# Kernel tuning notes

Measured on AMD Instinct MI355X. Metric: run time of the kernel, lower is better.

## Reference

```python
import jax, jax.numpy as jnp
import numpy as np

USER_NUM = 100000
ITEM_NUM = 100000
N_NODES = USER_NUM + ITEM_NUM
EMB = 64
N_EDGES = 6400000
N_LAYERS = 3
LAYER_CL = 1
EPS = 0.1


def setup_inputs() -> dict:
    key = jax.random.key(0)
    k1, k2, k3, k4, k5, k6 = jax.random.split(key, 6)
    # Xavier-uniform-like scale for embeddings
    scale = float(np.sqrt(6.0 / (USER_NUM + EMB)))
    user_emb = jax.random.normal(k1, (USER_NUM, EMB), dtype=jnp.float32) * scale
    item_emb = jax.random.normal(k2, (ITEM_NUM, EMB), dtype=jnp.float32) * scale
    adj_rows = jax.random.randint(k3, (N_EDGES,), 0, N_NODES, dtype=jnp.int64)
    adj_cols = jax.random.randint(k4, (N_EDGES,), 0, N_NODES, dtype=jnp.int64)
    # normalized adjacency values ~ 1/degree
    adj_vals = jax.random.uniform(k5, (N_EDGES,), dtype=jnp.float32) * (1.0 / 32.0)
    # precomputed uniform noise replacing torch.rand_like per layer
    noise = jax.random.uniform(k6, (N_LAYERS, N_NODES, EMB), dtype=jnp.float32)
    return {"user_emb": user_emb, "item_emb": item_emb, "adj_rows": adj_rows,
            "adj_cols": adj_cols, "adj_vals": adj_vals, "noise": noise}


def _spmm(rows, cols, vals, x):
    # sparse [N,N] @ dense [N,D] via gather + segment_sum
    return jax.ops.segment_sum(vals[:, None] * x[cols], rows, num_segments=N_NODES)


def reference(user_emb, item_emb, adj_rows, adj_cols, adj_vals, noise):
    ego = jnp.concatenate([user_emb, item_emb], axis=0)  # [N, D]
    cl = ego
    acc = jnp.zeros_like(ego)
    for k in range(N_LAYERS):
        ego = _spmm(adj_rows, adj_cols, adj_vals, ego)
        # perturbed branch: ego += sign(ego) * F.normalize(noise_k, dim=-1) * eps
        nk = noise[k]
        nrm = jnp.maximum(jnp.linalg.norm(nk, axis=-1, keepdims=True), 1e-12)
        ego = ego + jnp.sign(ego) * (nk / nrm) * EPS
        acc = acc + ego
        if k == LAYER_CL - 1:
            cl = ego
    final = acc / N_LAYERS  # mean over stacked layer outputs
    return (final[:USER_NUM], final[USER_NUM:], cl[:USER_NUM], cl[USER_NUM:])
```

## Files before the change

### kernel.cpp

```cpp
#include <hip/hip_runtime.h>


#define USER_NUM 100000
#define N_NODES  200000
#define EMB      64
#define N_EDGES  6400000
#define NBUCK    782
#define CAP      9216
#define EPB      16384
#define TB_A     1024
#define NBLK     391

static constexpr size_t BUFA_OFF  = 0;
static constexpr size_t BUFB_OFF  = 51200000;
static constexpr size_t CV_OFF    = 102400000;
static constexpr size_t RS_OFF    = 153600000;
static constexpr size_t SMALL_OFF = 154400016;
static constexpr size_t WS_NEED   = 156000016;

typedef float f4v __attribute__((ext_vector_type(4)));

__device__ __forceinline__ float4 ntload4(const float* p) {
    f4v v = __builtin_nontemporal_load((const f4v*)p);
    return make_float4(v.x, v.y, v.z, v.w);
}
__device__ __forceinline__ void ntstore4(float* p, float4 v) {
    f4v t = {v.x, v.y, v.z, v.w};
    __builtin_nontemporal_store(t, (f4v*)p);
}

__global__ __launch_bounds__(TB_A) void k_prep(const int* __restrict__ rows,
                                               const int* __restrict__ cols,
                                               const float* __restrict__ vals,
                                               int* __restrict__ bcnt_part,
                                               int2* __restrict__ zip) {
    __shared__ int h[NBUCK];
    for (int i = threadIdx.x; i < NBUCK; i += TB_A) h[i] = 0;
    __syncthreads();
    int base = blockIdx.x * EPB;
    int end  = min(base + EPB, N_EDGES);
    for (int e = base + threadIdx.x; e < end; e += TB_A) {
        atomicAdd(&h[rows[e] >> 8], 1);
        zip[e] = make_int2(cols[e], __float_as_int(vals[e]));
    }
    __syncthreads();
    for (int i = threadIdx.x; i < NBUCK; i += TB_A)
        bcnt_part[blockIdx.x * NBUCK + i] = h[i];
}

__global__ void k_scan782(const int* __restrict__ bcnt_part,
                          int* __restrict__ bcnt, int* __restrict__ bbase,
                          int* __restrict__ gcur, int* __restrict__ rs) {
    __shared__ int s[1024];
    int i = threadIdx.x;
    int v = 0;
    if (i < NBUCK) {
        for (int b = 0; b < NBLK; ++b) v += bcnt_part[b * NBUCK + i];
        bcnt[i] = v;
    }
    s[i] = v;
    __syncthreads();
    for (int off = 1; off < 1024; off <<= 1) {
        int t = 0;
        if (i >= off) t = s[i - off];
        __syncthreads();
        s[i] += t;
        __syncthreads();
    }
    if (i < NBUCK) {
        int ex = s[i] - v;
        bbase[i] = ex;
        gcur[i] = ex;
    }
    if (i == 0) rs[N_NODES] = N_EDGES;
}

__global__ __launch_bounds__(TB_A) void k_bin(const int* __restrict__ rows,
                                              int* __restrict__ gcur,
                                              int* __restrict__ keys) {
    __shared__ int h[NBUCK];
    __shared__ int gb[NBUCK];
    for (int i = threadIdx.x; i < NBUCK; i += TB_A) h[i] = 0;
    __syncthreads();
    int base = blockIdx.x * EPB;
    int end  = min(base + EPB, N_EDGES);
    for (int e = base + threadIdx.x; e < end; e += TB_A)
        atomicAdd(&h[rows[e] >> 8], 1);
    __syncthreads();
    for (int i = threadIdx.x; i < NBUCK; i += TB_A) {
        int c = h[i];
        gb[i] = c ? atomicAdd(&gcur[i], c) : 0;
        h[i] = 0;
    }
    __syncthreads();
    for (int e = base + threadIdx.x; e < end; e += TB_A) {
        int r = rows[e];
        int b = r >> 8;
        int pos = gb[b] + atomicAdd(&h[b], 1);
        keys[pos] = ((r & 255) << 24) | e;
    }
}

__global__ __launch_bounds__(256) void k_build(const int* __restrict__ keys,
                                               const int2* __restrict__ zip,
                                               const int* __restrict__ bcnt,
                                               const int* __restrict__ bbase,
                                               int2* __restrict__ cv,
                                               int* __restrict__ rs) {
    __shared__ int cnt[256];
    __shared__ int start[256];
    __shared__ int cur[256];
    __shared__ int scanbuf[256];
    __shared__ int eKey[CAP];
    int tid = threadIdx.x;
    int b = blockIdx.x;
    int n = bcnt[b];
    int base = bbase[b];
    int rowbase = b << 8;
    cnt[tid] = 0;
    __syncthreads();
    for (int i = tid; i < n; i += 256) {
        unsigned key = (unsigned)keys[base + i];
        atomicAdd(&cnt[key >> 24], 1);
    }
    __syncthreads();
    int v = cnt[tid];
    scanbuf[tid] = v;
    __syncthreads();
    for (int off = 1; off < 256; off <<= 1) {
        int t = 0;
        if (tid >= off) t = scanbuf[tid - off];
        __syncthreads();
        scanbuf[tid] += t;
        __syncthreads();
    }
    start[tid] = scanbuf[tid] - v;
    {
        int row = rowbase + tid;
        if (row < N_NODES) rs[row] = base + start[tid];
    }
    cur[tid] = 0;
    __syncthreads();
    if (n <= CAP) {
        for (int i = tid; i < n; i += 256) {
            int key = keys[base + i];
            int rl = (int)((unsigned)key >> 24);
            int p = start[rl] + atomicAdd(&cur[rl], 1);
            eKey[p] = key;
        }
        __syncthreads();
        for (int p = tid; p < n; p += 256) {
            int k = eKey[p];
            int rl = (int)((unsigned)k >> 24);
            int s0 = start[rl];
            int s1 = s0 + cnt[rl];
            int rank = 0;
            int q = s0;
            for (; q + 4 <= s1; q += 4) {
                rank += (eKey[q]     < k);
                rank += (eKey[q + 1] < k);
                rank += (eKey[q + 2] < k);
                rank += (eKey[q + 3] < k);
            }
            for (; q < s1; ++q) rank += (eKey[q] < k);
            int e = k & 0x00FFFFFF;
            cv[base + s0 + rank] = zip[e];
        }
    } else {
        for (int i = tid; i < n; i += 256) {
            int key = keys[base + i];
            int rl = (int)((unsigned)key >> 24);
            int p = start[rl] + atomicAdd(&cur[rl], 1);
            cv[base + p] = make_int2(key, 0);
        }
        __syncthreads();
        int c = cnt[tid];
        if (c > 1) {
            int s0 = start[tid];
            int s1 = s0 + c;
            for (int i = s0 + 1; i < s1; ++i) {
                int2 kv = cv[base + i];
                int j = i - 1;
                while (j >= s0 && cv[base + j].x > kv.x) {
                    cv[base + j + 1] = cv[base + j];
                    --j;
                }
                cv[base + j + 1] = kv;
            }
        }
        __syncthreads();
        for (int i = tid; i < n; i += 256) {
            int e = cv[base + i].x & 0x00FFFFFF;
            cv[base + i] = zip[e];
        }
    }
}

__global__ __launch_bounds__(256) void k_fused(const int* __restrict__ rs,
                                               const int2* __restrict__ cv,
                                               const float* __restrict__ xlo,
                                               const float* __restrict__ xhi,
                                               int split,
                                               const float* __restrict__ nk,
                                               float* __restrict__ ego,
                                               float* __restrict__ accF,
                                               float* __restrict__ clF,
                                               int mode) {
    int t = blockIdx.x * blockDim.x + threadIdx.x;
    int r = t >> 4;
    int u = t & 15;
    int c = u << 2;
    int idx = t << 2;
    float4 n4 = ntload4(nk + idx);
    float q0 = __fmul_rn(n4.x, n4.x);
    float q1 = __fmul_rn(n4.y, n4.y);
    float q2 = __fmul_rn(n4.z, n4.z);
    float q3 = __fmul_rn(n4.w, n4.w);
    float f0 = q0, f1 = q1, f2 = q2, f3 = q3;
    #pragma unroll
    for (int s = 0; s < 7; ++s) {
        float g0 = __shfl_up(f0, 2, 16);
        float g1 = __shfl_up(f1, 2, 16);
        float g2 = __shfl_up(f2, 2, 16);
        float g3 = __shfl_up(f3, 2, 16);
        if (u >= 2) {
            f0 = __fadd_rn(g0, q0);
            f1 = __fadd_rn(g1, q1);
            f2 = __fadd_rn(g2, q2);
            f3 = __fadd_rn(g3, q3);
        }
    }
    float tAB = __fadd_rn(__fadd_rn(f0, f1), __fadd_rn(f2, f3));
    float tlo = __shfl(tAB, 14, 16);
    float thi = __shfl(tAB, 15, 16);
    float nv = __fsqrt_rn(__fadd_rn(tlo, thi));
    nv = fmaxf(nv, 1e-12f);
    int j0 = rs[r], j1 = rs[r + 1];
    float a0 = 0.f, a1 = 0.f, a2 = 0.f, a3 = 0.f;
    if (j0 < j1) {
        const int EMAX = N_EDGES - 1;
        #define XROW(col) (((col) < split ? xlo : xhi) + \
                           ((col) < split ? (col) : (col) - split) * EMB + c)
        int2 c0 = cv[j0];
        int2 c1 = cv[min(j0 + 1, EMAX)];
        int2 c2 = cv[min(j0 + 2, EMAX)];
        int2 n0 = cv[min(j0 + 3, EMAX)];
        int2 n1 = cv[min(j0 + 4, EMAX)];
        int2 n2 = cv[min(j0 + 5, EMAX)];
        int2 m0 = cv[min(j0 + 6, EMAX)];
        int2 m1 = cv[min(j0 + 7, EMAX)];
        int2 m2 = cv[min(j0 + 8, EMAX)];
        float4 x0 = *(const float4*)XROW(c0.x);
        float4 x1 = *(const float4*)XROW(c1.x);
        float4 x2 = *(const float4*)XROW(c2.x);
        for (int j = j0; j < j1; j += 3) {
            float4 y0 = *(const float4*)XROW(n0.x);
            float4 y1 = *(const float4*)XROW(n1.x);
            float4 y2 = *(const float4*)XROW(n2.x);
            float v0 = __int_as_float(c0.y);
            float v1 = (j + 1 < j1) ? __int_as_float(c1.y) : 0.f;
            float v2 = (j + 2 < j1) ? __int_as_float(c2.y) : 0.f;
            a0 = __fadd_rn(a0, __fmul_rn(v0, x0.x));
            a1 = __fadd_rn(a1, __fmul_rn(v0, x0.y));
            a2 = __fadd_rn(a2, __fmul_rn(v0, x0.z));
            a3 = __fadd_rn(a3, __fmul_rn(v0, x0.w));
            a0 = __fadd_rn(a0, __fmul_rn(v1, x1.x));
            a1 = __fadd_rn(a1, __fmul_rn(v1, x1.y));
            a2 = __fadd_rn(a2, __fmul_rn(v1, x1.z));
            a3 = __fadd_rn(a3, __fmul_rn(v1, x1.w));
            a0 = __fadd_rn(a0, __fmul_rn(v2, x2.x));
            a1 = __fadd_rn(a1, __fmul_rn(v2, x2.y));
            a2 = __fadd_rn(a2, __fmul_rn(v2, x2.z));
            a3 = __fadd_rn(a3, __fmul_rn(v2, x2.w));
            c0 = n0; c1 = n1; c2 = n2;
            n0 = m0; n1 = m1; n2 = m2;
            x0 = y0; x1 = y1; x2 = y2;
            m0 = cv[min(j + 9,  EMAX)];
            m1 = cv[min(j + 10, EMAX)];
            m2 = cv[min(j + 11, EMAX)];
        }
        #undef XROW
    }
    float4 e4;
    {
        float s, q;
        s = (a0 > 0.f) ? 1.f : ((a0 < 0.f) ? -1.f : 0.f);
        q = __fdiv_rn(n4.x, nv);
        e4.x = __fadd_rn(a0, __fmul_rn(__fmul_rn(s, q), 0.1f));
        s = (a1 > 0.f) ? 1.f : ((a1 < 0.f) ? -1.f : 0.f);
        q = __fdiv_rn(n4.y, nv);
        e4.y = __fadd_rn(a1, __fmul_rn(__fmul_rn(s, q), 0.1f));
        s = (a2 > 0.f) ? 1.f : ((a2 < 0.f) ? -1.f : 0.f);
        q = __fdiv_rn(n4.z, nv);
        e4.z = __fadd_rn(a2, __fmul_rn(__fmul_rn(s, q), 0.1f));
        s = (a3 > 0.f) ? 1.f : ((a3 < 0.f) ? -1.f : 0.f);
        q = __fdiv_rn(n4.w, nv);
        e4.w = __fadd_rn(a3, __fmul_rn(__fmul_rn(s, q), 0.1f));
    }
    if (mode == 0) {
        ntstore4(clF + idx, e4);
    } else if (mode == 1) {
        ntstore4(ego + idx, e4);
    } else {
        float4 cl4 = ntload4(clF + idx);
        float4 x1 = *(const float4*)(xhi + idx);
        float4 a;
        a.x = __fadd_rn(cl4.x, x1.x);
        a.y = __fadd_rn(cl4.y, x1.y);
        a.z = __fadd_rn(cl4.z, x1.z);
        a.w = __fadd_rn(cl4.w, x1.w);
        float4 f;
        f.x = __fdiv_rn(__fadd_rn(a.x, e4.x), 3.0f);
        f.y = __fdiv_rn(__fadd_rn(a.y, e4.y), 3.0f);
        f.z = __fdiv_rn(__fadd_rn(a.z, e4.z), 3.0f);
        f.w = __fdiv_rn(__fadd_rn(a.w, e4.w), 3.0f);
        ntstore4(accF + idx, f);
    }
}

extern "C" void kernel_launch(void* const* d_in, const int* in_sizes, int n_in,
                              void* d_out, int out_size, void* d_ws, size_t ws_size,
                              hipStream_t stream) {
    if (ws_size < WS_NEED) return;

    const float* user_emb = (const float*)d_in[0];
    const float* item_emb = (const float*)d_in[1];
    const int*   adj_rows = (const int*)d_in[2];
    const int*   adj_cols = (const int*)d_in[3];
    const float* adj_vals = (const float*)d_in[4];
    const float* noise    = (const float*)d_in[5];

    char* ws = (char*)d_ws;
    float* bufB = (float*)(ws + BUFB_OFF);
    int*   keys = (int*)(ws + BUFA_OFF);
    int2*  zip  = (int2*)(ws + BUFB_OFF);
    int*   bcnt_part = (int*)(ws + CV_OFF);
    int2*  cv   = (int2*)(ws + CV_OFF);
    int*   rs   = (int*)(ws + RS_OFF);
    int*   bcnt = (int*)(ws + SMALL_OFF);
    int*   bbase= (int*)(ws + SMALL_OFF + 3200);
    int*   gcur = (int*)(ws + SMALL_OFF + 6400);

    float* accF = (float*)d_out;
    float* clF  = (float*)d_out + (size_t)N_NODES * EMB;

    k_prep<<<NBLK, TB_A, 0, stream>>>(adj_rows, adj_cols, adj_vals, bcnt_part,
                                      zip);
    k_scan782<<<1, 1024, 0, stream>>>(bcnt_part, bcnt, bbase, gcur, rs);
    k_bin<<<NBLK, TB_A, 0, stream>>>(adj_rows, gcur, keys);
    k_build<<<NBUCK, 256, 0, stream>>>(keys, zip, bcnt, bbase, cv, rs);

    const int T16 = N_NODES * 16;
    for (int k = 0; k < 3; ++k) {
        const float* nkp = noise + (size_t)k * N_NODES * EMB;
        const float* xlo  = (k == 0) ? user_emb : ((k == 1) ? clF : bufB);
        const float* xhi  = (k == 0) ? item_emb : ((k == 1) ? clF : bufB);
        int split = (k == 0) ? USER_NUM : 0;
        k_fused<<<T16 / 256, 256, 0, stream>>>(rs, cv, xlo, xhi, split,
                                               nkp, bufB, accF, clF, k);
    }
}
```

Before: 1.210 ms.

## Fold bucket scan into binning kernel with per-block prefix offsets

Removes the single-block scan kernel and has every binning block redundantly sum the per-block bucket histograms, scan the totals, and derive its own deterministic write offsets from the counts of earlier blocks. This drops one kernel launch, the global atomic cursor, and the second rows histogram pass in the binning kernel. In exchange, each of the 391 blocks now reads the whole 391x782 partial-count table, which adds redundant global reads and serial loop work per thread.

```diff
diff --git a/kernel.cpp b/kernel.cpp
--- a/kernel.cpp
+++ b/kernel.cpp
@@ -48,52 +48,48 @@
         bcnt_part[blockIdx.x * NBUCK + i] = h[i];
 }
 
-__global__ void k_scan782(const int* __restrict__ bcnt_part,
-                          int* __restrict__ bcnt, int* __restrict__ bbase,
-                          int* __restrict__ gcur, int* __restrict__ rs) {
+__global__ __launch_bounds__(TB_A) void k_bin(const int* __restrict__ rows,
+                                              const int* __restrict__ bcnt_part,
+                                              int* __restrict__ bcnt,
+                                              int* __restrict__ bbase,
+                                              int* __restrict__ rs,
+                                              int* __restrict__ keys) {
+    __shared__ int gb[NBUCK];
+    __shared__ int h[NBUCK];
     __shared__ int s[1024];
-    int i = threadIdx.x;
-    int v = 0;
-    if (i < NBUCK) {
-        for (int b = 0; b < NBLK; ++b) v += bcnt_part[b * NBUCK + i];
-        bcnt[i] = v;
-    }
-    s[i] = v;
+    int tid = threadIdx.x;
+    int blk = blockIdx.x;
+    int tot = 0, pre = 0;
+    if (tid < NBUCK) {
+        for (int b = 0; b < NBLK; ++b) {
+            int v = bcnt_part[b * NBUCK + tid];
+            tot += v;
+            if (b < blk) pre += v;
+        }
+    }
+    s[tid] = (tid < NBUCK) ? tot : 0;
     __syncthreads();
     for (int off = 1; off < 1024; off <<= 1) {
         int t = 0;
-        if (i >= off) t = s[i - off];
-        __syncthreads();
-        s[i] += t;
-        __syncthreads();
-    }
-    if (i < NBUCK) {
-        int ex = s[i] - v;
-        bbase[i] = ex;
-        gcur[i] = ex;
-    }
-    if (i == 0) rs[N_NODES] = N_EDGES;
-}
-
-__global__ __launch_bounds__(TB_A) void k_bin(const int* __restrict__ rows,
-                                              int* __restrict__ gcur,
-                                              int* __restrict__ keys) {
-    __shared__ int h[NBUCK];
-    __shared__ int gb[NBUCK];
-    for (int i = threadIdx.x; i < NBUCK; i += TB_A) h[i] = 0;
-    __syncthreads();
-    int base = blockIdx.x * EPB;
+        if (tid >= off) t = s[tid - off];
+        __syncthreads();
+        s[tid] += t;
+        __syncthreads();
+    }
+    if (tid < NBUCK) {
+        int ex = s[tid] - tot;
+        gb[tid] = ex + pre;
+        h[tid] = 0;
+        if (blk == 0) {
+            bcnt[tid] = tot;
+            bbase[tid] = ex;
+        }
+    }
+    if (blk == 0 && tid == 0) rs[N_NODES] = N_EDGES;
+    __syncthreads();
+    int base = blk * EPB;
     int end  = min(base + EPB, N_EDGES);
-    for (int e = base + threadIdx.x; e < end; e += TB_A)
-        atomicAdd(&h[rows[e] >> 8], 1);
-    __syncthreads();
-    for (int i = threadIdx.x; i < NBUCK; i += TB_A) {
-        int c = h[i];
-        gb[i] = c ? atomicAdd(&gcur[i], c) : 0;
-        h[i] = 0;
-    }
-    __syncthreads();
-    for (int e = base + threadIdx.x; e < end; e += TB_A) {
+    for (int e = base + tid; e < end; e += TB_A) {
         int r = rows[e];
         int b = r >> 8;
         int pos = gb[b] + atomicAdd(&h[b], 1);
@@ -339,15 +335,14 @@
     int*   rs   = (int*)(ws + RS_OFF);
     int*   bcnt = (int*)(ws + SMALL_OFF);
     int*   bbase= (int*)(ws + SMALL_OFF + 3200);
-    int*   gcur = (int*)(ws + SMALL_OFF + 6400);
 
     float* accF = (float*)d_out;
     float* clF  = (float*)d_out + (size_t)N_NODES * EMB;
 
     k_prep<<<NBLK, TB_A, 0, stream>>>(adj_rows, adj_cols, adj_vals, bcnt_part,
                                       zip);
-    k_scan782<<<1, 1024, 0, stream>>>(bcnt_part, bcnt, bbase, gcur, rs);
-    k_bin<<<NBLK, TB_A, 0, stream>>>(adj_rows, gcur, keys);
+    k_bin<<<NBLK, TB_A, 0, stream>>>(adj_rows, bcnt_part, bcnt, bbase, rs,
+                                     keys);
     k_build<<<NBUCK, 256, 0, stream>>>(keys, zip, bcnt, bbase, cv, rs);
 
     const int T16 = N_NODES * 16;
```

Measured after the change: 1.207 ms. No clear change (-0.3%).
